# Performance work log

Measured on AMD Instinct MI355X. Metric: run time of the kernel, lower is better.

## Reference

```python
import jax, jax.numpy as jnp
import numpy as np

LN_EPS = 1e-5

def _layer_norm(x, g, b):
    mu = jnp.mean(x, axis=-1, keepdims=True)
    var = jnp.mean(jnp.square(x - mu), axis=-1, keepdims=True)
    return (x - mu) * jax.lax.rsqrt(var + LN_EPS) * g + b

def _conv(x, src, tgt, N, alphas, ws, W3, W_self, bias, deg_power):
    # alphas, ws: tuples of 3 per-edge [E] arrays (sp, ctx, lat)
    # W3: [3, in, out]; deg_power: [3]
    out = x @ W_self + bias  # self loop + bias, [N, out]
    for c in range(3):
        eff = alphas[c] * ws[c]                                   # [E]
        deg = jnp.ones((N,), x.dtype).at[tgt].add(eff)            # [N]
        dinv = jnp.power(jnp.clip(deg, 1e-6), deg_power[c])       # [N]
        norm = eff * dinv[tgt] * dinv[src]                        # [E]
        h = x @ W3[c]                                             # [N, out] (linear => transform before gather)
        msg = norm[:, None] * h[src]                              # [E, out]
        out = out + jax.ops.segment_sum(msg, tgt, num_segments=N)
    return out

def setup_inputs() -> dict:
    N, E, D, L = 50000, 1000000, 128, 2
    key = jax.random.key(0)
    ks = jax.random.split(key, 16)
    scale = 1.0 / np.sqrt(D)
    inp = {
        "x": jax.random.normal(ks[0], (N, D), jnp.float32),
        "edge_index": jax.random.randint(ks[1], (2, E), 0, N, jnp.int32),
        "alpha_sp": jax.random.uniform(ks[2], (E,), jnp.float32),
        "alpha_ctx": jax.random.uniform(ks[3], (E,), jnp.float32),
        "alpha_lat": jax.random.uniform(ks[4], (E,), jnp.float32),
        "w_sp": jax.random.uniform(ks[5], (E,), jnp.float32),
        "w_ctx": jax.random.uniform(ks[6], (E,), jnp.float32),
        "w_lat": jax.random.uniform(ks[7], (E,), jnp.float32),
        # stacked per-layer params: [L, 3, in, out] for the three channel weights
        "W3": jax.random.normal(ks[8], (L, 3, D, D), jnp.float32) * scale,
        "W_self": jax.random.normal(ks[9], (L, D, D), jnp.float32) * scale,
        "bias": jnp.zeros((L, D), jnp.float32),
        "deg_power": jnp.full((L, 3), -0.5, jnp.float32),
        "ln_g": jnp.ones((D,), jnp.float32),
        "ln_b": jnp.zeros((D,), jnp.float32),
        "num_nodes": N,
    }
    return inp

def reference(x, edge_index, alpha_sp, alpha_ctx, alpha_lat, w_sp, w_ctx, w_lat,
              W3, W_self, bias, deg_power, ln_g, ln_b, num_nodes):
    N = num_nodes
    src, tgt = edge_index[0], edge_index[1]
    alphas = (alpha_sp, alpha_ctx, alpha_lat)
    ws = (w_sp, w_ctx, w_lat)
    L = W3.shape[0]
    h = x
    for i in range(L):
        h = _conv(h, src, tgt, N, alphas, ws, W3[i], W_self[i], bias[i], deg_power[i])
        if i < L - 1:
            h = _layer_norm(h, ln_g, ln_b)
            h = jax.nn.relu(h)
            # dropout: eval mode (identity)
    return h
```

## Files before the change

### kernel.cpp

```cpp
#include <hip/hip_runtime.h>
#include <hip/hip_bf16.h>

typedef short bf16x8 __attribute__((ext_vector_type(8)));
typedef float f32x4 __attribute__((ext_vector_type(4)));

#define BSH 7
#define BK  (1 << BSH)

static inline int cdiv(int a, int b){ return (a + b - 1) / b; }

__device__ __forceinline__ unsigned pack_bf16_hi(float v){
    return ((unsigned)__bfloat16_as_ushort(__float2bfloat16(v))) << 16;
}
__device__ __forceinline__ float bf16hi_to_f32(unsigned bits_hi16){
    return __uint_as_float(bits_hi16);
}

__global__ __launch_bounds__(256) void k_bcnt0(const int* __restrict__ tgt,
                                               int* __restrict__ gcnt, int E, int NB){
    __shared__ int lh[1024];
    int tid = threadIdx.x;
    for (int b = tid; b < 1024; b += 256) lh[b] = 0;
    __syncthreads();
    int c0 = blockIdx.x * 4096;
    #pragma unroll
    for (int u = 0; u < 16; ++u){
        int e = c0 + u * 256 + tid;
        if (e < E) atomicAdd(&lh[tgt[e] >> BSH], 1);
    }
    __syncthreads();
    for (int b = tid; b < NB; b += 256){
        int c = lh[b];
        if (c) atomicAdd(&gcnt[b], c);
    }
}

__global__ __launch_bounds__(256) void k_bscan(const int* __restrict__ gcnt,
                                               int* __restrict__ bbase,
                                               int* __restrict__ gcur,
                                               int* __restrict__ rs,
                                               int N, int E){
    __shared__ int sc[256];
    int tid = threadIdx.x;
    int b0 = tid * 4;
    int v0 = gcnt[b0], v1 = gcnt[b0 + 1], v2 = gcnt[b0 + 2], v3 = gcnt[b0 + 3];
    int t3 = v0 + v1 + v2 + v3;
    sc[tid] = t3;
    __syncthreads();
    for (int off = 1; off < 256; off <<= 1){
        int x = (tid >= off) ? sc[tid - off] : 0;
        __syncthreads();
        sc[tid] += x;
        __syncthreads();
    }
    int ex = sc[tid] - t3;
    bbase[b0]     = ex;
    bbase[b0 + 1] = ex + v0;
    bbase[b0 + 2] = ex + v0 + v1;
    bbase[b0 + 3] = ex + v0 + v1 + v2;
    gcur[b0] = bbase[b0]; gcur[b0 + 1] = bbase[b0 + 1];
    gcur[b0 + 2] = bbase[b0 + 2]; gcur[b0 + 3] = bbase[b0 + 3];
    if (tid == 255) bbase[1024] = sc[255];
    if (tid == 0)   rs[N] = E;
}

__global__ __launch_bounds__(256) void k_bin(
        const int* __restrict__ src, const int* __restrict__ tgt,
        const float* __restrict__ asp, const float* __restrict__ actx,
        const float* __restrict__ alat, const float* __restrict__ wsp,
        const float* __restrict__ wctx, const float* __restrict__ wlat,
        int* __restrict__ gcur, uint4* __restrict__ binned, int E, int NB){
    __shared__ int lh[1024], lc[1024], gb[1024];
    int tid = threadIdx.x;
    int c0 = blockIdx.x * 4096;
    for (int b = tid; b < 1024; b += 256){ lh[b] = 0; lc[b] = 0; }
    __syncthreads();
    #pragma unroll
    for (int u = 0; u < 16; ++u){
        int e = c0 + u * 256 + tid;
        if (e < E) atomicAdd(&lh[tgt[e] >> BSH], 1);
    }
    __syncthreads();
    for (int b = tid; b < NB; b += 256){
        int c = lh[b];
        gb[b] = c ? atomicAdd(&gcur[b], c) : 0;
    }
    __syncthreads();
    #pragma unroll
    for (int u = 0; u < 16; ++u){
        int e = c0 + u * 256 + tid;
        if (e < E){
            int t = tgt[e];
            int b = t >> BSH;
            int p = gb[b] + atomicAdd(&lc[b], 1);
            uint4 o;
            o.x = (unsigned)src[e] | pack_bf16_hi(asp[e] * wsp[e]);
            o.y = (pack_bf16_hi(actx[e] * wctx[e]) >> 16) | pack_bf16_hi(alat[e] * wlat[e]);
            o.z = (unsigned)t;
            o.w = 0u;
            binned[p] = o;
        }
    }
}

__global__ __launch_bounds__(256) void k_bucket(
        const uint4* __restrict__ binned, const int* __restrict__ bbase,
        const float* __restrict__ dp,
        uint2* __restrict__ effo, int* __restrict__ rs,
        float* __restrict__ dinv_all,
        int N, int L){
    __shared__ int th[128], sc2[128], cur[128];
    __shared__ float sm[384];
    int tid = threadIdx.x;
    int b = blockIdx.x;
    int t0 = b << BSH;
    int ebeg = bbase[b], eend = bbase[b + 1];
    if (tid < 128) th[tid] = 0;
    for (int j = tid; j < 384; j += 256) sm[j] = 0.f;
    __syncthreads();
    for (int i = ebeg + tid; i < eend; i += 256)
        atomicAdd(&th[(int)binned[i].z - t0], 1);
    __syncthreads();
    int v = (tid < 128) ? th[tid] : 0;
    if (tid < 128) sc2[tid] = v;
    __syncthreads();
    for (int off = 1; off < 128; off <<= 1){
        int x = (tid >= off && tid < 128) ? sc2[tid - off] : 0;
        __syncthreads();
        if (tid < 128) sc2[tid] += x;
        __syncthreads();
    }
    if (tid < 128){
        int exv = sc2[tid] - v;
        cur[tid] = exv;
        int t = t0 + tid;
        if (t < N) rs[t] = ebeg + exv;
    }
    __syncthreads();
    for (int i = ebeg + tid; i < eend; i += 256){
        uint4 r = binned[i];
        int loc = (int)r.z - t0;
        int p = atomicAdd(&cur[loc], 1);
        uint2 o = {r.x, r.y};
        effo[ebeg + p] = o;
        atomicAdd(&sm[loc * 3 + 0], bf16hi_to_f32(r.x & 0xFFFF0000u));
        atomicAdd(&sm[loc * 3 + 1], bf16hi_to_f32(r.y << 16));
        atomicAdd(&sm[loc * 3 + 2], bf16hi_to_f32(r.y & 0xFFFF0000u));
    }
    __syncthreads();
    if (tid < 128){
        int t = t0 + tid;
        if (t < N){
            float d0 = fmaxf(1.f + sm[tid * 3 + 0], 1e-6f);
            float d1 = fmaxf(1.f + sm[tid * 3 + 1], 1e-6f);
            float d2 = fmaxf(1.f + sm[tid * 3 + 2], 1e-6f);
            for (int l = 0; l < L; ++l){
                size_t base = ((size_t)l * N + t) * 3;
                dinv_all[base + 0] = powf(d0, dp[l * 3 + 0]);
                dinv_all[base + 1] = powf(d1, dp[l * 3 + 1]);
                dinv_all[base + 2] = powf(d2, dp[l * 3 + 2]);
            }
        }
    }
}

__global__ void k_normv(const uint2* __restrict__ effo,
                        const float* __restrict__ dinv_all,
                        uint2* __restrict__ nv, int E, int N, int L){
    int i = blockIdx.x * 256 + threadIdx.x;
    if (i >= L * E) return;
    int l = i / E;
    int e = i - l * E;
    const float* dinv = dinv_all + (size_t)l * N * 3;
    uint2 v = effo[e];
    unsigned s = v.x & 0xFFFFu;
    float e0 = bf16hi_to_f32(v.x & 0xFFFF0000u);
    float e1 = bf16hi_to_f32(v.y << 16);
    float e2 = bf16hi_to_f32(v.y & 0xFFFF0000u);
    float n0 = e0 * dinv[3 * s + 0];
    float n1 = e1 * dinv[3 * s + 1];
    float n2 = e2 * dinv[3 * s + 2];
    uint2 o;
    o.x = s | pack_bf16_hi(n0);
    o.y = (pack_bf16_hi(n1) >> 16) | pack_bf16_hi(n2);
    nv[i] = o;
}

__global__ void k_prep(const float* __restrict__ x, __hip_bfloat16* __restrict__ xg,
                       const float* __restrict__ Wself, const float* __restrict__ W3,
                       __hip_bfloat16* __restrict__ BT, int nx, int nw){
    int i = blockIdx.x * 256 + threadIdx.x;
    if (i < nx){
        xg[i] = __float2bfloat16(x[i]);
    } else {
        int q = i - nx;
        if (q < nw){
            int l = q >> 16, r = q & 65535;
            int j = r >> 9, k = r & 511;
            float v;
            if (k < 128) v = Wself[l * 16384 + k * 128 + j];
            else {
                int c = (k >> 7) - 1, kk = k & 127;
                v = W3[l * 49152 + (c * 128 + kk) * 128 + j];
            }
            BT[q] = __float2bfloat16(v);
        }
    }
}

__global__ __launch_bounds__(256) void k_msg(
        const __hip_bfloat16* __restrict__ xg,
        __hip_bfloat16* __restrict__ Yg,
        const uint2* __restrict__ nv,
        const int* __restrict__ rs,
        const float* __restrict__ dinv,
        int N){
    int w = threadIdx.x >> 6, lane = threadIdx.x & 63;
    int t = blockIdx.x * 4 + w;
    if (t >= N) return;
    float ax0 = 0.f, ay0 = 0.f, ax1 = 0.f, ay1 = 0.f, ax2 = 0.f, ay2 = 0.f;
    int beg = rs[t], end = rs[t + 1];
    int i = beg;
    for (; i + 8 <= end; i += 8){
        uint2 m[8];
        #pragma unroll
        for (int u = 0; u < 8; ++u) m[u] = nv[i + u];
        float2 f[8];
        #pragma unroll
        for (int u = 0; u < 8; ++u){
            const __hip_bfloat162* p =
                (const __hip_bfloat162*)(xg + (size_t)(m[u].x & 0xFFFFu) * 128);
            f[u] = __bfloat1622float2(p[lane]);
        }
        #pragma unroll
        for (int u = 0; u < 8; ++u){
            float n0 = bf16hi_to_f32(m[u].x & 0xFFFF0000u);
            float n1 = bf16hi_to_f32(m[u].y << 16);
            float n2 = bf16hi_to_f32(m[u].y & 0xFFFF0000u);
            ax0 += n0 * f[u].x; ay0 += n0 * f[u].y;
            ax1 += n1 * f[u].x; ay1 += n1 * f[u].y;
            ax2 += n2 * f[u].x; ay2 += n2 * f[u].y;
        }
    }
    for (; i < end; ++i){
        uint2 m = nv[i];
        const __hip_bfloat162* p =
            (const __hip_bfloat162*)(xg + (size_t)(m.x & 0xFFFFu) * 128);
        float2 fv = __bfloat1622float2(p[lane]);
        float n0 = bf16hi_to_f32(m.x & 0xFFFF0000u);
        float n1 = bf16hi_to_f32(m.y << 16);
        float n2 = bf16hi_to_f32(m.y & 0xFFFF0000u);
        ax0 += n0 * fv.x; ay0 += n0 * fv.y;
        ax1 += n1 * fv.x; ay1 += n1 * fv.y;
        ax2 += n2 * fv.x; ay2 += n2 * fv.y;
    }
    float dt0 = dinv[3 * t], dt1 = dinv[3 * t + 1], dt2 = dinv[3 * t + 2];
    __hip_bfloat162* yo = (__hip_bfloat162*)(Yg + (size_t)t * 384) + lane;
    float2 r0 = {dt0 * ax0, dt0 * ay0};
    float2 r1 = {dt1 * ax1, dt1 * ay1};
    float2 r2 = {dt2 * ax2, dt2 * ay2};
    yo[0]   = __float22bfloat162_rn(r0);
    yo[64]  = __float22bfloat162_rn(r1);
    yo[128] = __float22bfloat162_rn(r2);
}

__global__ __launch_bounds__(256) void k_gemm(
        const __hip_bfloat16* __restrict__ Yg,
        const __hip_bfloat16* __restrict__ BT,
        const float* __restrict__ bias,
        float* __restrict__ outbuf,
        int M, int doLN,
        const float* __restrict__ g, const float* __restrict__ b,
        __hip_bfloat16* __restrict__ xg){
    __shared__ __hip_bfloat16 As[128 * 128];
    __shared__ __hip_bfloat16 Bs[128 * 128];
    const int tid = threadIdx.x;
    const int row0 = blockIdx.x * 128;
    const int w = tid >> 6, lane = tid & 63;
    const int wm = (w & 1) * 64, wn = (w >> 1) * 64;
    const int lm = lane & 15, lq = lane >> 4;

    f32x4 acc[4][4];
    #pragma unroll
    for (int mt = 0; mt < 4; ++mt)
        #pragma unroll
        for (int nt = 0; nt < 4; ++nt)
            acc[mt][nt] = {0.f, 0.f, 0.f, 0.f};

    for (int kt = 0; kt < 4; ++kt){
        #pragma unroll
        for (int it = 0; it < 8; ++it){
            int v = it * 256 + tid;
            int r = v >> 4, c = v & 15;
            int soff = r * 128 + ((c ^ (r & 15)) << 3);
            int4 av = {0, 0, 0, 0};
            if (row0 + r < M){
                if (kt == 0)
                    av = *(const int4*)(xg + (size_t)(row0 + r) * 128 + (c << 3));
                else
                    av = *(const int4*)(Yg + (size_t)(row0 + r) * 384
                                        + (kt - 1) * 128 + (c << 3));
            }
            *(int4*)(&As[soff]) = av;
            int4 bv = *(const int4*)(BT + (size_t)r * 512 + kt * 128 + (c << 3));
            *(int4*)(&Bs[soff]) = bv;
        }
        __syncthreads();

        #pragma unroll
        for (int kk = 0; kk < 4; ++kk){
            int kc = kk * 4 + lq;
            bf16x8 a[4], b2[4];
            #pragma unroll
            for (int mt = 0; mt < 4; ++mt){
                int r = wm + mt * 16 + lm;
                a[mt] = *(const bf16x8*)(&As[r * 128 + ((kc ^ (r & 15)) << 3)]);
            }
            #pragma unroll
            for (int nt = 0; nt < 4; ++nt){
                int r = wn + nt * 16 + lm;
                b2[nt] = *(const bf16x8*)(&Bs[r * 128 + ((kc ^ (r & 15)) << 3)]);
            }
            #pragma unroll
            for (int mt = 0; mt < 4; ++mt)
                #pragma unroll
                for (int nt = 0; nt < 4; ++nt)
                    acc[mt][nt] = __builtin_amdgcn_mfma_f32_16x16x32_bf16(
                        a[mt], b2[nt], acc[mt][nt], 0, 0, 0);
        }
        __syncthreads();
    }

    if (!doLN){
        #pragma unroll
        for (int mt = 0; mt < 4; ++mt){
            #pragma unroll
            for (int nt = 0; nt < 4; ++nt){
                int col = wn + nt * 16 + lm;
                #pragma unroll
                for (int r = 0; r < 4; ++r){
                    int row = row0 + wm + mt * 16 + lq * 4 + r;
                    if (row < M)
                        outbuf[(size_t)row * 128 + col] = acc[mt][nt][r] + bias[col];
                }
            }
        }
    } else {
        float* S1 = (float*)As;
        float* S2 = S1 + 4096;
        float* MS = (float*)Bs;
        const int half = wn >> 6;
        const int slot = half * 16 + lm;
        float bv[4];
        #pragma unroll
        for (int nt = 0; nt < 4; ++nt) bv[nt] = bias[wn + nt * 16 + lm];
        #pragma unroll
        for (int mt = 0; mt < 4; ++mt){
            #pragma unroll
            for (int r = 0; r < 4; ++r){
                int rl = wm + mt * 16 + lq * 4 + r;
                float ps = 0.f, pq = 0.f;
                #pragma unroll
                for (int nt = 0; nt < 4; ++nt){
                    float v = acc[mt][nt][r] + bv[nt];
                    ps += v; pq += v * v;
                }
                S1[rl * 32 + slot] = ps;
                S2[rl * 32 + slot] = pq;
            }
        }
        __syncthreads();
        if (tid < 128){
            float s = 0.f, sq = 0.f;
            #pragma unroll
            for (int j = 0; j < 32; ++j){
                s  += S1[tid * 32 + j];
                sq += S2[tid * 32 + j];
            }
            float mu = s * (1.0f / 128.0f);
            float var = sq * (1.0f / 128.0f) - mu * mu;
            MS[tid] = mu;
            MS[128 + tid] = rsqrtf(var + 1e-5f);
        }
        __syncthreads();
        float gv[4], bbv[4];
        #pragma unroll
        for (int nt = 0; nt < 4; ++nt){
            int col = wn + nt * 16 + lm;
            gv[nt] = g[col]; bbv[nt] = b[col];
        }
        #pragma unroll
        for (int mt = 0; mt < 4; ++mt){
            #pragma unroll
            for (int r = 0; r < 4; ++r){
                int rl = wm + mt * 16 + lq * 4 + r;
                int row = row0 + rl;
                if (row < M){
                    float mu = MS[rl], sc = MS[128 + rl];
                    #pragma unroll
                    for (int nt = 0; nt < 4; ++nt){
                        int col = wn + nt * 16 + lm;
                        float v = acc[mt][nt][r] + bv[nt];
                        float y = fmaxf((v - mu) * sc * gv[nt] + bbv[nt], 0.0f);
                        xg[(size_t)row * 128 + col] = __float2bfloat16(y);
                    }
                }
            }
        }
    }
}

extern "C" void kernel_launch(void* const* d_in, const int* in_sizes, int n_in,
                              void* d_out, int out_size, void* d_ws, size_t ws_size,
                              hipStream_t stream) {
    const float* x     = (const float*)d_in[0];
    const int*   ei    = (const int*)d_in[1];
    const float* asp   = (const float*)d_in[2];
    const float* actx  = (const float*)d_in[3];
    const float* alat  = (const float*)d_in[4];
    const float* wsp   = (const float*)d_in[5];
    const float* wctx  = (const float*)d_in[6];
    const float* wlat  = (const float*)d_in[7];
    const float* W3    = (const float*)d_in[8];
    const float* Wself = (const float*)d_in[9];
    const float* bias  = (const float*)d_in[10];
    const float* dpow  = (const float*)d_in[11];
    const float* lng   = (const float*)d_in[12];
    const float* lnb   = (const float*)d_in[13];

    const int N = in_sizes[0] / 128;
    const int E = in_sizes[1] / 2;
    const int L = in_sizes[8] / (3 * 128 * 128);
    const int NB = cdiv(N, BK);
    const int* src = ei;
    const int* tgt = ei + E;

    char* p = (char*)d_ws;
    auto alloc = [&](size_t bytes) -> void* {
        void* r = (void*)p;
        p += (bytes + 255) & ~(size_t)255;
        return r;
    };
    int*   rs       = (int*)  alloc((size_t)(N + 1) * 4);
    int*   gcnt     = (int*)  alloc(1024 * 4);
    int*   bbase    = (int*)  alloc(1025 * 4);
    int*   gcur     = (int*)  alloc(1024 * 4);
    uint2* effo     = (uint2*)alloc((size_t)E * 8);
    size_t nv_bytes = (size_t)L * E * 8, bn_bytes = (size_t)E * 16;
    uint2* nv       = (uint2*)alloc(nv_bytes > bn_bytes ? nv_bytes : bn_bytes);
    float* dinv_all = (float*)alloc((size_t)L * N * 3 * 4);
    __hip_bfloat16* xg = (__hip_bfloat16*)alloc((size_t)N * 128 * 2);
    __hip_bfloat16* Yg = (__hip_bfloat16*)alloc((size_t)N * 384 * 2);
    __hip_bfloat16* BT = (__hip_bfloat16*)alloc((size_t)L * 128 * 512 * 2);
    uint4* binned = (uint4*)nv;

    hipMemsetAsync(gcnt, 0, 1024 * 4, stream);
    k_bcnt0 <<<cdiv(E, 4096), 256, 0, stream>>>(tgt, gcnt, E, NB);
    k_bscan <<<1, 256, 0, stream>>>(gcnt, bbase, gcur, rs, N, E);
    k_bin   <<<cdiv(E, 4096), 256, 0, stream>>>(src, tgt, asp, actx, alat, wsp, wctx, wlat,
                                                gcur, binned, E, NB);
    k_bucket<<<NB, 256, 0, stream>>>(binned, bbase, dpow, effo, rs, dinv_all, N, L);
    k_normv <<<cdiv(L * E, 256), 256, 0, stream>>>(effo, dinv_all, nv, E, N, L);
    {
        int nx = N * 128, nw = L * 65536;
        k_prep<<<cdiv(nx + nw, 256), 256, 0, stream>>>(x, xg, Wself, W3, BT, nx, nw);
    }

    for (int l = 0; l < L; ++l){
        int doLN = (l < L - 1) ? 1 : 0;
        const float* dinv_l = dinv_all + (size_t)l * N * 3;
        k_msg <<<cdiv(N, 4), 256, 0, stream>>>(xg, Yg, nv + (size_t)l * E, rs, dinv_l, N);
        k_gemm<<<cdiv(N, 128), 256, 0, stream>>>(Yg, BT + (size_t)l * 65536,
                                                 bias + l * 128, (float*)d_out, N,
                                                 doLN, lng, lnb, xg);
    }
}
```

Before: 351.7 us.

## Fuse CSR preprocessing kernels into one cooperative kernel with grid syncs

Merges the memset, bucket count, scan, binning, per-bucket sort/degree, norm-value and input/weight conversion kernels into a single cooperative launch separated by grid.sync barriers. The aim is to remove several kernel launch gaps and the separate memset. The grid is sized max(NB, chunks), about 391 blocks, which must all be co-resident for the cooperative launch to work. Each phase then loops over its work with a block stride. The float-to-bf16 conversion of x is also vectorised to float4 loads.

```diff
diff --git a/kernel.cpp b/kernel.cpp
--- a/kernel.cpp
+++ b/kernel.cpp
@@ -1,5 +1,8 @@
 #include <hip/hip_runtime.h>
 #include <hip/hip_bf16.h>
+#include <hip/hip_cooperative_groups.h>
+
+namespace cg = cooperative_groups;
 
 typedef short bf16x8 __attribute__((ext_vector_type(8)));
 typedef float f32x4 __attribute__((ext_vector_type(4)));
@@ -16,185 +19,189 @@
     return __uint_as_float(bits_hi16);
 }
 
-__global__ __launch_bounds__(256) void k_bcnt0(const int* __restrict__ tgt,
-                                               int* __restrict__ gcnt, int E, int NB){
-    __shared__ int lh[1024];
-    int tid = threadIdx.x;
-    for (int b = tid; b < 1024; b += 256) lh[b] = 0;
-    __syncthreads();
-    int c0 = blockIdx.x * 4096;
-    #pragma unroll
-    for (int u = 0; u < 16; ++u){
-        int e = c0 + u * 256 + tid;
-        if (e < E) atomicAdd(&lh[tgt[e] >> BSH], 1);
-    }
-    __syncthreads();
-    for (int b = tid; b < NB; b += 256){
-        int c = lh[b];
-        if (c) atomicAdd(&gcnt[b], c);
-    }
-}
-
-__global__ __launch_bounds__(256) void k_bscan(const int* __restrict__ gcnt,
-                                               int* __restrict__ bbase,
-                                               int* __restrict__ gcur,
-                                               int* __restrict__ rs,
-                                               int N, int E){
-    __shared__ int sc[256];
-    int tid = threadIdx.x;
-    int b0 = tid * 4;
-    int v0 = gcnt[b0], v1 = gcnt[b0 + 1], v2 = gcnt[b0 + 2], v3 = gcnt[b0 + 3];
-    int t3 = v0 + v1 + v2 + v3;
-    sc[tid] = t3;
-    __syncthreads();
-    for (int off = 1; off < 256; off <<= 1){
-        int x = (tid >= off) ? sc[tid - off] : 0;
-        __syncthreads();
-        sc[tid] += x;
-        __syncthreads();
-    }
-    int ex = sc[tid] - t3;
-    bbase[b0]     = ex;
-    bbase[b0 + 1] = ex + v0;
-    bbase[b0 + 2] = ex + v0 + v1;
-    bbase[b0 + 3] = ex + v0 + v1 + v2;
-    gcur[b0] = bbase[b0]; gcur[b0 + 1] = bbase[b0 + 1];
-    gcur[b0 + 2] = bbase[b0 + 2]; gcur[b0 + 3] = bbase[b0 + 3];
-    if (tid == 255) bbase[1024] = sc[255];
-    if (tid == 0)   rs[N] = E;
-}
-
-__global__ __launch_bounds__(256) void k_bin(
+__global__ __launch_bounds__(256) void k_coprep(
         const int* __restrict__ src, const int* __restrict__ tgt,
         const float* __restrict__ asp, const float* __restrict__ actx,
         const float* __restrict__ alat, const float* __restrict__ wsp,
         const float* __restrict__ wctx, const float* __restrict__ wlat,
-        int* __restrict__ gcur, uint4* __restrict__ binned, int E, int NB){
-    __shared__ int lh[1024], lc[1024], gb[1024];
-    int tid = threadIdx.x;
-    int c0 = blockIdx.x * 4096;
-    for (int b = tid; b < 1024; b += 256){ lh[b] = 0; lc[b] = 0; }
-    __syncthreads();
-    #pragma unroll
-    for (int u = 0; u < 16; ++u){
-        int e = c0 + u * 256 + tid;
-        if (e < E) atomicAdd(&lh[tgt[e] >> BSH], 1);
-    }
-    __syncthreads();
-    for (int b = tid; b < NB; b += 256){
-        int c = lh[b];
-        gb[b] = c ? atomicAdd(&gcur[b], c) : 0;
-    }
-    __syncthreads();
-    #pragma unroll
-    for (int u = 0; u < 16; ++u){
-        int e = c0 + u * 256 + tid;
-        if (e < E){
-            int t = tgt[e];
-            int b = t >> BSH;
-            int p = gb[b] + atomicAdd(&lc[b], 1);
-            uint4 o;
-            o.x = (unsigned)src[e] | pack_bf16_hi(asp[e] * wsp[e]);
-            o.y = (pack_bf16_hi(actx[e] * wctx[e]) >> 16) | pack_bf16_hi(alat[e] * wlat[e]);
-            o.z = (unsigned)t;
-            o.w = 0u;
-            binned[p] = o;
-        }
-    }
-}
-
-__global__ __launch_bounds__(256) void k_bucket(
-        const uint4* __restrict__ binned, const int* __restrict__ bbase,
-        const float* __restrict__ dp,
-        uint2* __restrict__ effo, int* __restrict__ rs,
-        float* __restrict__ dinv_all,
-        int N, int L){
-    __shared__ int th[128], sc2[128], cur[128];
-    __shared__ float sm[384];
-    int tid = threadIdx.x;
-    int b = blockIdx.x;
-    int t0 = b << BSH;
-    int ebeg = bbase[b], eend = bbase[b + 1];
-    if (tid < 128) th[tid] = 0;
-    for (int j = tid; j < 384; j += 256) sm[j] = 0.f;
-    __syncthreads();
-    for (int i = ebeg + tid; i < eend; i += 256)
-        atomicAdd(&th[(int)binned[i].z - t0], 1);
-    __syncthreads();
-    int v = (tid < 128) ? th[tid] : 0;
-    if (tid < 128) sc2[tid] = v;
-    __syncthreads();
-    for (int off = 1; off < 128; off <<= 1){
-        int x = (tid >= off && tid < 128) ? sc2[tid - off] : 0;
-        __syncthreads();
-        if (tid < 128) sc2[tid] += x;
-        __syncthreads();
-    }
-    if (tid < 128){
-        int exv = sc2[tid] - v;
-        cur[tid] = exv;
-        int t = t0 + tid;
-        if (t < N) rs[t] = ebeg + exv;
-    }
-    __syncthreads();
-    for (int i = ebeg + tid; i < eend; i += 256){
-        uint4 r = binned[i];
-        int loc = (int)r.z - t0;
-        int p = atomicAdd(&cur[loc], 1);
-        uint2 o = {r.x, r.y};
-        effo[ebeg + p] = o;
-        atomicAdd(&sm[loc * 3 + 0], bf16hi_to_f32(r.x & 0xFFFF0000u));
-        atomicAdd(&sm[loc * 3 + 1], bf16hi_to_f32(r.y << 16));
-        atomicAdd(&sm[loc * 3 + 2], bf16hi_to_f32(r.y & 0xFFFF0000u));
-    }
-    __syncthreads();
-    if (tid < 128){
-        int t = t0 + tid;
-        if (t < N){
-            float d0 = fmaxf(1.f + sm[tid * 3 + 0], 1e-6f);
-            float d1 = fmaxf(1.f + sm[tid * 3 + 1], 1e-6f);
-            float d2 = fmaxf(1.f + sm[tid * 3 + 2], 1e-6f);
-            for (int l = 0; l < L; ++l){
-                size_t base = ((size_t)l * N + t) * 3;
-                dinv_all[base + 0] = powf(d0, dp[l * 3 + 0]);
-                dinv_all[base + 1] = powf(d1, dp[l * 3 + 1]);
-                dinv_all[base + 2] = powf(d2, dp[l * 3 + 2]);
-            }
-        }
-    }
-}
-
-__global__ void k_normv(const uint2* __restrict__ effo,
-                        const float* __restrict__ dinv_all,
-                        uint2* __restrict__ nv, int E, int N, int L){
-    int i = blockIdx.x * 256 + threadIdx.x;
-    if (i >= L * E) return;
-    int l = i / E;
-    int e = i - l * E;
-    const float* dinv = dinv_all + (size_t)l * N * 3;
-    uint2 v = effo[e];
-    unsigned s = v.x & 0xFFFFu;
-    float e0 = bf16hi_to_f32(v.x & 0xFFFF0000u);
-    float e1 = bf16hi_to_f32(v.y << 16);
-    float e2 = bf16hi_to_f32(v.y & 0xFFFF0000u);
-    float n0 = e0 * dinv[3 * s + 0];
-    float n1 = e1 * dinv[3 * s + 1];
-    float n2 = e2 * dinv[3 * s + 2];
-    uint2 o;
-    o.x = s | pack_bf16_hi(n0);
-    o.y = (pack_bf16_hi(n1) >> 16) | pack_bf16_hi(n2);
-    nv[i] = o;
-}
-
-__global__ void k_prep(const float* __restrict__ x, __hip_bfloat16* __restrict__ xg,
-                       const float* __restrict__ Wself, const float* __restrict__ W3,
-                       __hip_bfloat16* __restrict__ BT, int nx, int nw){
-    int i = blockIdx.x * 256 + threadIdx.x;
-    if (i < nx){
-        xg[i] = __float2bfloat16(x[i]);
-    } else {
-        int q = i - nx;
-        if (q < nw){
+        const float* __restrict__ dp, const float* __restrict__ x,
+        const float* __restrict__ Wself, const float* __restrict__ W3,
+        int* __restrict__ gcnt, int* __restrict__ bbase, int* __restrict__ gcur,
+        int* __restrict__ rs, uint2* __restrict__ effo, uint2* __restrict__ nv,
+        float* __restrict__ dinv_all, __hip_bfloat16* __restrict__ xg,
+        __hip_bfloat16* __restrict__ BT,
+        int N, int E, int L, int NB){
+    cg::grid_group grid = cg::this_grid();
+    __shared__ int sm0[1024], sm1[1024], sm2[1024];
+    const int tid = threadIdx.x, bid = blockIdx.x, nblk = gridDim.x;
+    const int nch = (E + 4095) >> 12;
+    uint4* binned = (uint4*)nv;
+
+    if (bid == 0) for (int b = tid; b < 1024; b += 256) gcnt[b] = 0;
+    grid.sync();
+
+    for (int ch = bid; ch < nch; ch += nblk){
+        for (int b = tid; b < 1024; b += 256) sm0[b] = 0;
+        __syncthreads();
+        int c0 = ch << 12;
+        #pragma unroll
+        for (int u = 0; u < 16; ++u){
+            int e = c0 + u * 256 + tid;
+            if (e < E) atomicAdd(&sm0[tgt[e] >> BSH], 1);
+        }
+        __syncthreads();
+        for (int b = tid; b < NB; b += 256){
+            int c = sm0[b];
+            if (c) atomicAdd(&gcnt[b], c);
+        }
+        __syncthreads();
+    }
+    grid.sync();
+
+    if (bid == 0){
+        int b0 = tid * 4;
+        int v0 = gcnt[b0], v1 = gcnt[b0 + 1], v2 = gcnt[b0 + 2], v3 = gcnt[b0 + 3];
+        int t3 = v0 + v1 + v2 + v3;
+        sm0[tid] = t3;
+        __syncthreads();
+        for (int off = 1; off < 256; off <<= 1){
+            int xx = (tid >= off) ? sm0[tid - off] : 0;
+            __syncthreads();
+            sm0[tid] += xx;
+            __syncthreads();
+        }
+        int ex = sm0[tid] - t3;
+        bbase[b0]     = ex;
+        bbase[b0 + 1] = ex + v0;
+        bbase[b0 + 2] = ex + v0 + v1;
+        bbase[b0 + 3] = ex + v0 + v1 + v2;
+        gcur[b0] = bbase[b0]; gcur[b0 + 1] = bbase[b0 + 1];
+        gcur[b0 + 2] = bbase[b0 + 2]; gcur[b0 + 3] = bbase[b0 + 3];
+        if (tid == 255) bbase[1024] = sm0[255];
+        if (tid == 0)   rs[N] = E;
+    }
+    grid.sync();
+
+    for (int ch = bid; ch < nch; ch += nblk){
+        int* lh = sm0; int* lc = sm1; int* gb = sm2;
+        for (int b = tid; b < 1024; b += 256){ lh[b] = 0; lc[b] = 0; }
+        __syncthreads();
+        int c0 = ch << 12;
+        #pragma unroll
+        for (int u = 0; u < 16; ++u){
+            int e = c0 + u * 256 + tid;
+            if (e < E) atomicAdd(&lh[tgt[e] >> BSH], 1);
+        }
+        __syncthreads();
+        for (int b = tid; b < NB; b += 256){
+            int c = lh[b];
+            gb[b] = c ? atomicAdd(&gcur[b], c) : 0;
+        }
+        __syncthreads();
+        #pragma unroll
+        for (int u = 0; u < 16; ++u){
+            int e = c0 + u * 256 + tid;
+            if (e < E){
+                int t = tgt[e];
+                int b = t >> BSH;
+                int p = gb[b] + atomicAdd(&lc[b], 1);
+                uint4 o;
+                o.x = (unsigned)src[e] | pack_bf16_hi(asp[e] * wsp[e]);
+                o.y = (pack_bf16_hi(actx[e] * wctx[e]) >> 16) | pack_bf16_hi(alat[e] * wlat[e]);
+                o.z = (unsigned)t;
+                o.w = 0u;
+                binned[p] = o;
+            }
+        }
+        __syncthreads();
+    }
+    grid.sync();
+
+    for (int b = bid; b < NB; b += nblk){
+        int* th  = sm0;
+        int* sc2 = sm0 + 128;
+        int* cur = sm0 + 256;
+        float* smf = (float*)sm1;
+        int t0 = b << BSH;
+        int ebeg = bbase[b], eend = bbase[b + 1];
+        if (tid < 128) th[tid] = 0;
+        for (int j = tid; j < 384; j += 256) smf[j] = 0.f;
+        __syncthreads();
+        for (int i = ebeg + tid; i < eend; i += 256)
+            atomicAdd(&th[(int)binned[i].z - t0], 1);
+        __syncthreads();
+        int v = (tid < 128) ? th[tid] : 0;
+        if (tid < 128) sc2[tid] = v;
+        __syncthreads();
+        for (int off = 1; off < 128; off <<= 1){
+            int xx = (tid >= off && tid < 128) ? sc2[tid - off] : 0;
+            __syncthreads();
+            if (tid < 128) sc2[tid] += xx;
+            __syncthreads();
+        }
+        if (tid < 128){
+            int exv = sc2[tid] - v;
+            cur[tid] = exv;
+            int t = t0 + tid;
+            if (t < N) rs[t] = ebeg + exv;
+        }
+        __syncthreads();
+        for (int i = ebeg + tid; i < eend; i += 256){
+            uint4 r = binned[i];
+            int loc = (int)r.z - t0;
+            int p = atomicAdd(&cur[loc], 1);
+            uint2 o = {r.x, r.y};
+            effo[ebeg + p] = o;
+            atomicAdd(&smf[loc * 3 + 0], bf16hi_to_f32(r.x & 0xFFFF0000u));
+            atomicAdd(&smf[loc * 3 + 1], bf16hi_to_f32(r.y << 16));
+            atomicAdd(&smf[loc * 3 + 2], bf16hi_to_f32(r.y & 0xFFFF0000u));
+        }
+        __syncthreads();
+        if (tid < 128){
+            int t = t0 + tid;
+            if (t < N){
+                float d0 = fmaxf(1.f + smf[tid * 3 + 0], 1e-6f);
+                float d1 = fmaxf(1.f + smf[tid * 3 + 1], 1e-6f);
+                float d2 = fmaxf(1.f + smf[tid * 3 + 2], 1e-6f);
+                for (int l = 0; l < L; ++l){
+                    size_t base = ((size_t)l * N + t) * 3;
+                    dinv_all[base + 0] = powf(d0, dp[l * 3 + 0]);
+                    dinv_all[base + 1] = powf(d1, dp[l * 3 + 1]);
+                    dinv_all[base + 2] = powf(d2, dp[l * 3 + 2]);
+                }
+            }
+        }
+        __syncthreads();
+    }
+    grid.sync();
+
+    {
+        const int gstride = nblk * 256;
+        const int gidx = bid * 256 + tid;
+        for (int i = gidx; i < L * E; i += gstride){
+            int l = i / E;
+            int e = i - l * E;
+            const float* dinv = dinv_all + (size_t)l * N * 3;
+            uint2 vv = effo[e];
+            unsigned s = vv.x & 0xFFFFu;
+            float e0 = bf16hi_to_f32(vv.x & 0xFFFF0000u);
+            float e1 = bf16hi_to_f32(vv.y << 16);
+            float e2 = bf16hi_to_f32(vv.y & 0xFFFF0000u);
+            uint2 o;
+            o.x = s | pack_bf16_hi(e0 * dinv[3 * s + 0]);
+            o.y = (pack_bf16_hi(e1 * dinv[3 * s + 1]) >> 16)
+                | pack_bf16_hi(e2 * dinv[3 * s + 2]);
+            nv[i] = o;
+        }
+        int nx4 = (N * 128) >> 2;
+        for (int i = gidx; i < nx4; i += gstride){
+            float4 v = ((const float4*)x)[i];
+            float2 lo = {v.x, v.y}, hi = {v.z, v.w};
+            ((__hip_bfloat162*)xg)[2 * i]     = __float22bfloat162_rn(lo);
+            ((__hip_bfloat162*)xg)[2 * i + 1] = __float22bfloat162_rn(hi);
+        }
+        int nw = L * 65536;
+        for (int q = gidx; q < nw; q += gstride){
             int l = q >> 16, r = q & 65535;
             int j = r >> 9, k = r & 511;
             float v;
@@ -428,10 +435,10 @@
     const float* lng   = (const float*)d_in[12];
     const float* lnb   = (const float*)d_in[13];
 
-    const int N = in_sizes[0] / 128;
-    const int E = in_sizes[1] / 2;
-    const int L = in_sizes[8] / (3 * 128 * 128);
-    const int NB = cdiv(N, BK);
+    int N = in_sizes[0] / 128;
+    int E = in_sizes[1] / 2;
+    int L = in_sizes[8] / (3 * 128 * 128);
+    int NB = cdiv(N, BK);
     const int* src = ei;
     const int* tgt = ei + E;
 
@@ -452,18 +459,18 @@
     __hip_bfloat16* xg = (__hip_bfloat16*)alloc((size_t)N * 128 * 2);
     __hip_bfloat16* Yg = (__hip_bfloat16*)alloc((size_t)N * 384 * 2);
     __hip_bfloat16* BT = (__hip_bfloat16*)alloc((size_t)L * 128 * 512 * 2);
-    uint4* binned = (uint4*)nv;
-
-    hipMemsetAsync(gcnt, 0, 1024 * 4, stream);
-    k_bcnt0 <<<cdiv(E, 4096), 256, 0, stream>>>(tgt, gcnt, E, NB);
-    k_bscan <<<1, 256, 0, stream>>>(gcnt, bbase, gcur, rs, N, E);
-    k_bin   <<<cdiv(E, 4096), 256, 0, stream>>>(src, tgt, asp, actx, alat, wsp, wctx, wlat,
-                                                gcur, binned, E, NB);
-    k_bucket<<<NB, 256, 0, stream>>>(binned, bbase, dpow, effo, rs, dinv_all, N, L);
-    k_normv <<<cdiv(L * E, 256), 256, 0, stream>>>(effo, dinv_all, nv, E, N, L);
+
     {
-        int nx = N * 128, nw = L * 65536;
-        k_prep<<<cdiv(nx + nw, 256), 256, 0, stream>>>(x, xg, Wself, W3, BT, nx, nw);
+        int nch = cdiv(E, 4096);
+        int gblocks = NB > nch ? NB : nch;
+        void* kargs[] = {
+            (void*)&src, (void*)&tgt, (void*)&asp, (void*)&actx, (void*)&alat,
+            (void*)&wsp, (void*)&wctx, (void*)&wlat, (void*)&dpow, (void*)&x,
+            (void*)&Wself, (void*)&W3, (void*)&gcnt, (void*)&bbase, (void*)&gcur,
+            (void*)&rs, (void*)&effo, (void*)&nv, (void*)&dinv_all, (void*)&xg,
+            (void*)&BT, (void*)&N, (void*)&E, (void*)&L, (void*)&NB };
+        hipLaunchCooperativeKernel((void*)k_coprep, dim3(gblocks), dim3(256),
+                                   kargs, 0, stream);
     }
 
     for (int l = 0; l < L; ++l){
```

Result: slower. 570.5 us (+62.2%).
